# Kernel optimization log

Measured on AMD Instinct MI355X. Metric: run time of the kernel, lower is better.

## Reference

```python
import jax, jax.numpy as jnp
import numpy as np

N = 50000
E = 800000
IN_C = 128
HID = 64
HEADS = 4
OUT_C = 64


def setup_inputs() -> dict:
    key = jax.random.key(0)
    ks = jax.random.split(key, 20)
    s = 0.05
    inp = {
        "x": jax.random.normal(ks[0], (N, IN_C), dtype=jnp.float32),
        "edge_index": jax.random.randint(ks[1], (2, E), 0, N, dtype=jnp.int64),
        # layer 0: in=128 -> heads=4, C=64
        "W0": jax.random.normal(ks[2], (IN_C, HEADS * HID), jnp.float32) * s,
        "a0s": jax.random.normal(ks[3], (HEADS, HID), jnp.float32) * s,
        "a0d": jax.random.normal(ks[4], (HEADS, HID), jnp.float32) * s,
        "b0": jnp.zeros((HEADS * HID,), jnp.float32),
        # layer 1: 256 -> heads=4, C=64
        "W1": jax.random.normal(ks[5], (HEADS * HID, HEADS * HID), jnp.float32) * s,
        "a1s": jax.random.normal(ks[6], (HEADS, HID), jnp.float32) * s,
        "a1d": jax.random.normal(ks[7], (HEADS, HID), jnp.float32) * s,
        "b1": jnp.zeros((HEADS * HID,), jnp.float32),
        # layer 2: 256 -> heads=1, C=64
        "W2": jax.random.normal(ks[8], (HEADS * HID, HID), jnp.float32) * s,
        "a2s": jax.random.normal(ks[9], (1, HID), jnp.float32) * s,
        "a2d": jax.random.normal(ks[10], (1, HID), jnp.float32) * s,
        "b2": jnp.zeros((HID,), jnp.float32),
        # prediction head: Linear(64 -> 64)
        "hw": jax.random.normal(ks[11], (HID, OUT_C), jnp.float32) * s,
        "hb": jnp.zeros((OUT_C,), jnp.float32),
    }
    return inp


def gat_conv(x, src, dst, W, a_s, a_d, b, heads, n_nodes):
    # x: [N, F_in]; returns [N, heads*C]
    C = a_s.shape[1]
    h = (x @ W).reshape(n_nodes, heads, C)          # [N,H,C]
    alpha_s = jnp.sum(h * a_s, axis=-1)             # [N,H]
    alpha_d = jnp.sum(h * a_d, axis=-1)             # [N,H]
    e = jax.nn.leaky_relu(alpha_s[src] + alpha_d[dst], negative_slope=0.2)  # [E,H]
    m = jax.ops.segment_max(e, dst, num_segments=n_nodes)                  # per-dst max
    ex = jnp.exp(e - m[dst])
    denom = jax.ops.segment_sum(ex, dst, num_segments=n_nodes)
    alpha = ex / (denom[dst] + 1e-16)               # [E,H]
    out = jax.ops.segment_sum(alpha[:, :, None] * h[src], dst, num_segments=n_nodes)
    return out.reshape(n_nodes, heads * C) + b


def reference(x, edge_index, W0, a0s, a0d, b0, W1, a1s, a1d, b1, W2, a2s, a2d, b2, hw, hb):
    n = x.shape[0]
    # PyG GATConv default add_self_loops=True
    loop = jnp.arange(n, dtype=edge_index.dtype)
    src = jnp.concatenate([edge_index[0], loop])
    dst = jnp.concatenate([edge_index[1], loop])

    h = gat_conv(x, src, dst, W0, a0s, a0d, b0, HEADS, n)
    h = jax.nn.relu(h)
    h = gat_conv(h, src, dst, W1, a1s, a1d, b1, HEADS, n)
    h = jax.nn.relu(h)
    h = gat_conv(h, src, dst, W2, a2s, a2d, b2, 1, n)
    # batch is None -> mean over all nodes, keepdim
    g = jnp.mean(h, axis=0, keepdims=True)          # [1, HID]
    return g @ hw + hb                               # [1, OUT_C]
```

## Files before the change

### kernel.cpp

```cpp
#include <hip/hip_runtime.h>
#include <hip/hip_bf16.h>
#include <cstddef>

#define NN 50000
#define EE 800000

typedef __attribute__((ext_vector_type(8))) short short8;
typedef __attribute__((ext_vector_type(4))) float f32x4;

#define GLB __attribute__((address_space(1)))
#define LDS __attribute__((address_space(3)))

__device__ __forceinline__ float leaky(float x) { return x >= 0.f ? x : 0.2f * x; }
__device__ __forceinline__ float bf2f(unsigned short u) {
  return __uint_as_float(((unsigned int)u) << 16);
}
__device__ __forceinline__ float bflo(unsigned int v) { return __uint_as_float(v << 16); }
__device__ __forceinline__ float bfhi(unsigned int v) { return __uint_as_float(v & 0xFFFF0000u); }
__device__ __forceinline__ unsigned short f2bf(float f) {
  __hip_bfloat16 b = __float2bfloat16(f);
  return __builtin_bit_cast(unsigned short, b);
}
__device__ __forceinline__ void accum8(float a, uint4 v, float* acc) {
  acc[0] += a * bflo(v.x); acc[1] += a * bfhi(v.x);
  acc[2] += a * bflo(v.y); acc[3] += a * bfhi(v.y);
  acc[4] += a * bflo(v.z); acc[5] += a * bfhi(v.z);
  acc[6] += a * bflo(v.w); acc[7] += a * bfhi(v.w);
}

template <int LAYER>
__global__ __launch_bounds__(256) void gemm128_k(const unsigned short* __restrict__ A,
                                                 const unsigned short* __restrict__ Bt,
                                                 unsigned short* __restrict__ Cb,
                                                 int K,
                                                 const float* __restrict__ a_s,
                                                 const float* __restrict__ a_d,
                                                 float* __restrict__ als,
                                                 float* __restrict__ ald,
                                                 float* __restrict__ selfex) {
  __shared__ __align__(16) unsigned short As[4][64 * 32];
  __shared__ __align__(16) unsigned short Bs[4][128 * 32];
  const int tid = threadIdx.x;
  const int lane = tid & 63;
  const int w = tid >> 6;
  const int bm = blockIdx.x * 64;
  const int bn = blockIdx.y * 128;
  const int quad = lane >> 4;
  const int l16 = lane & 15;
  const int lrow = lane >> 2;
  const int lseg = lane & 3;
  f32x4 acc[8] = {};

  for (int kv = 0; kv < K; kv += 128) {
    if (kv) __syncthreads();
#pragma unroll
    for (int ks = 0; ks < 4; ++ks) {
      const int kc = kv + ks * 32;
      {
        int row = w * 16 + lrow;
        int g = lseg ^ ((row >> 2) & 3);
        int sr = bm + row; if (sr >= NN) sr = NN - 1;
        const unsigned short* gp = A + (size_t)sr * K + kc + g * 8;
        __builtin_amdgcn_global_load_lds((const GLB void*)gp,
                                         (LDS void*)&As[ks][(w * 16) * 32], 16, 0, 0);
      }
#pragma unroll
      for (int c = 0; c < 2; ++c) {
        int row = w * 32 + c * 16 + lrow;
        int g = lseg ^ ((row >> 2) & 3);
        const unsigned short* gp = Bt + (size_t)(bn + row) * K + kc + g * 8;
        __builtin_amdgcn_global_load_lds((const GLB void*)gp,
                                         (LDS void*)&Bs[ks][(w * 32 + c * 16) * 32], 16, 0, 0);
      }
    }
    __syncthreads();
#pragma unroll
    for (int ks = 0; ks < 4; ++ks) {
      const int ra = w * 16 + l16;
      short8 afr = *(const short8*)&As[ks][ra * 32 + ((quad ^ ((ra >> 2) & 3)) << 3)];
#pragma unroll
      for (int nt = 0; nt < 8; ++nt) {
        int rb = nt * 16 + l16;
        short8 bfr = *(const short8*)&Bs[ks][rb * 32 + ((quad ^ ((rb >> 2) & 3)) << 3)];
        acc[nt] = __builtin_amdgcn_mfma_f32_16x16x32_bf16(afr, bfr, acc[nt], 0, 0, 0);
      }
    }
  }
  const int h0 = blockIdx.y * 2;
  float vs[2][4] = {};
  float vd[2][4] = {};
#pragma unroll
  for (int nt = 0; nt < 8; ++nt) {
    const int h = nt >> 2;
    const float asv = a_s[(h0 + h) * 64 + (nt & 3) * 16 + l16];
    const float adv = a_d[(h0 + h) * 64 + (nt & 3) * 16 + l16];
#pragma unroll
    for (int reg = 0; reg < 4; ++reg) {
      unsigned short c = f2bf(acc[nt][reg]);
      int r = bm + w * 16 + quad * 4 + reg;
      if (r < NN) Cb[(size_t)r * 256 + bn + nt * 16 + l16] = c;
      float hv = bf2f(c);
      vs[h][reg] += hv * asv;
      vd[h][reg] += hv * adv;
    }
  }
#pragma unroll
  for (int off = 1; off < 16; off <<= 1) {
#pragma unroll
    for (int h = 0; h < 2; ++h)
#pragma unroll
      for (int reg = 0; reg < 4; ++reg) {
        vs[h][reg] += __shfl_xor(vs[h][reg], off, 64);
        vd[h][reg] += __shfl_xor(vd[h][reg], off, 64);
      }
  }
  if (l16 == 0) {
#pragma unroll
    for (int reg = 0; reg < 4; ++reg) {
      int r = bm + w * 16 + quad * 4 + reg;
      if (r < NN) {
#pragma unroll
        for (int h = 0; h < 2; ++h) {
          als[(size_t)r * 4 + h0 + h] = vs[h][reg];
          ald[(size_t)r * 4 + h0 + h] = vd[h][reg];
          selfex[(size_t)r * 4 + h0 + h] = __expf(leaky(vs[h][reg] + vd[h][reg]));
        }
      }
    }
  }
}

__global__ __launch_bounds__(256) void gemm64v_k(const unsigned short* __restrict__ A,
                                                 const unsigned short* __restrict__ Bt,
                                                 unsigned short* __restrict__ Cb,
                                                 int K,
                                                 const float* __restrict__ a_s,
                                                 const float* __restrict__ a_d,
                                                 float* __restrict__ als,
                                                 float* __restrict__ ald,
                                                 float* __restrict__ selfex) {
  __shared__ __align__(16) unsigned short As[4][64 * 32];
  __shared__ __align__(16) unsigned short Bs[4][64 * 32];
  const int tid = threadIdx.x;
  const int lane = tid & 63;
  const int w = tid >> 6;
  const int bm = blockIdx.x * 64;
  const int quad = lane >> 4;
  const int l16 = lane & 15;
  const int lrow = lane >> 2;
  const int lseg = lane & 3;
  f32x4 acc[4] = {};

  for (int kv = 0; kv < K; kv += 128) {
    if (kv) __syncthreads();
#pragma unroll
    for (int ks = 0; ks < 4; ++ks) {
      const int kc = kv + ks * 32;
      {
        int row = w * 16 + lrow;
        int g = lseg ^ ((row >> 2) & 3);
        int sr = bm + row; if (sr >= NN) sr = NN - 1;
        const unsigned short* gp = A + (size_t)sr * K + kc + g * 8;
        __builtin_amdgcn_global_load_lds((const GLB void*)gp,
                                         (LDS void*)&As[ks][(w * 16) * 32], 16, 0, 0);
      }
      {
        int row = w * 16 + lrow;
        int g = lseg ^ ((row >> 2) & 3);
        const unsigned short* gp = Bt + (size_t)row * K + kc + g * 8;
        __builtin_amdgcn_global_load_lds((const GLB void*)gp,
                                         (LDS void*)&Bs[ks][(w * 16) * 32], 16, 0, 0);
      }
    }
    __syncthreads();
#pragma unroll
    for (int ks = 0; ks < 4; ++ks) {
      const int ra = w * 16 + l16;
      short8 afr = *(const short8*)&As[ks][ra * 32 + ((quad ^ ((ra >> 2) & 3)) << 3)];
#pragma unroll
      for (int nt = 0; nt < 4; ++nt) {
        int rb = nt * 16 + l16;
        short8 bfr = *(const short8*)&Bs[ks][rb * 32 + ((quad ^ ((rb >> 2) & 3)) << 3)];
        acc[nt] = __builtin_amdgcn_mfma_f32_16x16x32_bf16(afr, bfr, acc[nt], 0, 0, 0);
      }
    }
  }
  float vs[4] = {};
  float vd[4] = {};
#pragma unroll
  for (int nt = 0; nt < 4; ++nt) {
    const float asv = a_s[nt * 16 + l16];
    const float adv = a_d[nt * 16 + l16];
#pragma unroll
    for (int reg = 0; reg < 4; ++reg) {
      unsigned short c = f2bf(acc[nt][reg]);
      int r = bm + w * 16 + quad * 4 + reg;
      if (r < NN) Cb[(size_t)r * 64 + nt * 16 + l16] = c;
      float hv = bf2f(c);
      vs[reg] += hv * asv;
      vd[reg] += hv * adv;
    }
  }
#pragma unroll
  for (int off = 1; off < 16; off <<= 1) {
#pragma unroll
    for (int reg = 0; reg < 4; ++reg) {
      vs[reg] += __shfl_xor(vs[reg], off, 64);
      vd[reg] += __shfl_xor(vd[reg], off, 64);
    }
  }
  if (l16 == 0) {
#pragma unroll
    for (int reg = 0; reg < 4; ++reg) {
      int r = bm + w * 16 + quad * 4 + reg;
      if (r < NN) {
        als[r] = vs[reg];
        ald[r] = vd[reg];
        selfex[r] = __expf(leaky(vs[reg] + vd[reg]));
      }
    }
  }
}

__global__ __launch_bounds__(256) void aggr4c_k(const int* __restrict__ deg,
                                                const int* __restrict__ csr_src,
                                                const float* __restrict__ als,
                                                const float* __restrict__ ald,
                                                const float* __restrict__ selfex,
                                                const uint4* __restrict__ hb4,
                                                const float* __restrict__ bias,
                                                uint4* __restrict__ out4) {
  const int dst = blockIdx.x * 4 + (threadIdx.x >> 6);
  const int lane = threadIdx.x & 63;
  const int slot = lane >> 4;
  const int l16 = lane & 15;
  const int head = l16 >> 2;
  const int rs = dst << 6;
  int dg = deg[dst]; dg = dg < 64 ? dg : 64;
  const float aldv = ald[dst * 4 + head];

  float acc[16] = {};
  float dsum = 0.f;
  if (slot == 0) {
    float a = selfex[dst * 4 + head];
    dsum += a;
    uint4 v0 = hb4[(size_t)dst * 32 + l16 * 2];
    uint4 v1 = hb4[(size_t)dst * 32 + l16 * 2 + 1];
    accum8(a, v0, acc);
    accum8(a, v1, acc + 8);
  }
  int j = slot;
  for (; j + 4 < dg; j += 8) {
    int s0 = csr_src[rs + j];
    int s1 = csr_src[rs + j + 4];
    float e0 = als[s0 * 4 + head];
    float e1 = als[s1 * 4 + head];
    uint4 va0 = hb4[(size_t)s0 * 32 + l16 * 2];
    uint4 vb0 = hb4[(size_t)s0 * 32 + l16 * 2 + 1];
    uint4 va1 = hb4[(size_t)s1 * 32 + l16 * 2];
    uint4 vb1 = hb4[(size_t)s1 * 32 + l16 * 2 + 1];
    float a0 = __expf(leaky(e0 + aldv));
    float a1 = __expf(leaky(e1 + aldv));
    dsum += a0 + a1;
    accum8(a0, va0, acc);
    accum8(a0, vb0, acc + 8);
    accum8(a1, va1, acc);
    accum8(a1, vb1, acc + 8);
  }
  for (; j < dg; j += 4) {
    int s0 = csr_src[rs + j];
    float e0 = als[s0 * 4 + head];
    uint4 va0 = hb4[(size_t)s0 * 32 + l16 * 2];
    uint4 vb0 = hb4[(size_t)s0 * 32 + l16 * 2 + 1];
    float a0 = __expf(leaky(e0 + aldv));
    dsum += a0;
    accum8(a0, va0, acc);
    accum8(a0, vb0, acc + 8);
  }
#pragma unroll
  for (int k = 0; k < 16; ++k) {
    acc[k] += __shfl_xor(acc[k], 16, 64);
    acc[k] += __shfl_xor(acc[k], 32, 64);
  }
  dsum += __shfl_xor(dsum, 16, 64);
  dsum += __shfl_xor(dsum, 32, 64);
  if (slot == 0) {
    const float inv = 1.f / (dsum + 1e-16f);
    const float* bz = bias + l16 * 16;
    uint4 o0, o1;
    float c0, c1;
    c0 = fmaxf(acc[0] * inv + bz[0], 0.f);   c1 = fmaxf(acc[1] * inv + bz[1], 0.f);
    o0.x = ((unsigned int)f2bf(c1) << 16) | f2bf(c0);
    c0 = fmaxf(acc[2] * inv + bz[2], 0.f);   c1 = fmaxf(acc[3] * inv + bz[3], 0.f);
    o0.y = ((unsigned int)f2bf(c1) << 16) | f2bf(c0);
    c0 = fmaxf(acc[4] * inv + bz[4], 0.f);   c1 = fmaxf(acc[5] * inv + bz[5], 0.f);
    o0.z = ((unsigned int)f2bf(c1) << 16) | f2bf(c0);
    c0 = fmaxf(acc[6] * inv + bz[6], 0.f);   c1 = fmaxf(acc[7] * inv + bz[7], 0.f);
    o0.w = ((unsigned int)f2bf(c1) << 16) | f2bf(c0);
    c0 = fmaxf(acc[8] * inv + bz[8], 0.f);   c1 = fmaxf(acc[9] * inv + bz[9], 0.f);
    o1.x = ((unsigned int)f2bf(c1) << 16) | f2bf(c0);
    c0 = fmaxf(acc[10] * inv + bz[10], 0.f); c1 = fmaxf(acc[11] * inv + bz[11], 0.f);
    o1.y = ((unsigned int)f2bf(c1) << 16) | f2bf(c0);
    c0 = fmaxf(acc[12] * inv + bz[12], 0.f); c1 = fmaxf(acc[13] * inv + bz[13], 0.f);
    o1.z = ((unsigned int)f2bf(c1) << 16) | f2bf(c0);
    c0 = fmaxf(acc[14] * inv + bz[14], 0.f); c1 = fmaxf(acc[15] * inv + bz[15], 0.f);
    o1.w = ((unsigned int)f2bf(c1) << 16) | f2bf(c0);
    out4[(size_t)dst * 32 + l16 * 2] = o0;
    out4[(size_t)dst * 32 + l16 * 2 + 1] = o1;
  }
}

__global__ __launch_bounds__(256) void aggr1c_k(const int* __restrict__ deg,
                                                const int* __restrict__ csr_src,
                                                const float* __restrict__ als,
                                                const float* __restrict__ ald,
                                                const float* __restrict__ selfex,
                                                const uint4* __restrict__ hb4,
                                                const float* __restrict__ bias,
                                                float* __restrict__ out) {
  const int dst = blockIdx.x * 4 + (threadIdx.x >> 6);
  const int lane = threadIdx.x & 63;
  const int slot = lane >> 3;
  const int c8 = lane & 7;
  const int rs = dst << 6;
  int dg = deg[dst]; dg = dg < 64 ? dg : 64;
  const float aldv = ald[dst];

  float acc[8] = {};
  float dsum = 0.f;
  if (slot == 0) {
    float a = selfex[dst];
    dsum += a;
    uint4 v = hb4[(size_t)dst * 8 + c8];
    accum8(a, v, acc);
  }
  int j = slot;
  for (; j + 8 < dg; j += 16) {
    int s0 = csr_src[rs + j];
    int s1 = csr_src[rs + j + 8];
    float e0 = als[s0];
    float e1 = als[s1];
    uint4 v0 = hb4[(size_t)s0 * 8 + c8];
    uint4 v1 = hb4[(size_t)s1 * 8 + c8];
    float a0 = __expf(leaky(e0 + aldv));
    float a1 = __expf(leaky(e1 + aldv));
    dsum += a0 + a1;
    accum8(a0, v0, acc);
    accum8(a1, v1, acc);
  }
  for (; j < dg; j += 8) {
    int s = csr_src[rs + j];
    float e = als[s];
    uint4 v = hb4[(size_t)s * 8 + c8];
    float a = __expf(leaky(e + aldv));
    dsum += a;
    accum8(a, v, acc);
  }
#pragma unroll
  for (int k = 0; k < 8; ++k) {
    acc[k] += __shfl_xor(acc[k], 8, 64);
    acc[k] += __shfl_xor(acc[k], 16, 64);
    acc[k] += __shfl_xor(acc[k], 32, 64);
  }
  dsum += __shfl_xor(dsum, 8, 64);
  dsum += __shfl_xor(dsum, 16, 64);
  dsum += __shfl_xor(dsum, 32, 64);
  if (slot == 0) {
    const float inv = 1.f / (dsum + 1e-16f);
    const float4 bz0 = *(const float4*)(bias + c8 * 8);
    const float4 bz1 = *(const float4*)(bias + c8 * 8 + 4);
    float4 o0 = make_float4(acc[0] * inv + bz0.x, acc[1] * inv + bz0.y,
                            acc[2] * inv + bz0.z, acc[3] * inv + bz0.w);
    float4 o1 = make_float4(acc[4] * inv + bz1.x, acc[5] * inv + bz1.y,
                            acc[6] * inv + bz1.z, acc[7] * inv + bz1.w);
    *(float4*)(out + (size_t)dst * 64 + c8 * 8) = o0;
    *(float4*)(out + (size_t)dst * 64 + c8 * 8 + 4) = o1;
  }
}

#define HS_BLK 782
__global__ __launch_bounds__(256) void prep_k(const int* __restrict__ ei,
                                              int* __restrict__ deg,
                                              int* __restrict__ csr_src,
                                              const float2* __restrict__ x2,
                                              unsigned int* __restrict__ xb_u,
                                              const float* __restrict__ W0,
                                              unsigned short* __restrict__ W0t,
                                              const float* __restrict__ W1,
                                              unsigned short* __restrict__ W1t,
                                              const float* __restrict__ W2,
                                              unsigned short* __restrict__ W2t,
                                              float* __restrict__ g) {
  int bid = blockIdx.x;
  int tid = threadIdx.x;
  if (bid < HS_BLK) {
    const int base = bid * 1024 + tid;
    int ss[4], dd[4], jj[4];
#pragma unroll
    for (int k = 0; k < 4; ++k) {
      int i = base + k * 256;
      bool m = i < EE;
      ss[k] = m ? ei[i] : 0;
      dd[k] = m ? ei[EE + i] : 0;
      jj[k] = 64;
      if (m) jj[k] = atomicAdd(&deg[dd[k]], 1);
    }
#pragma unroll
    for (int k = 0; k < 4; ++k)
      if (jj[k] < 64) csr_src[(dd[k] << 6) + jj[k]] = ss[k];
    return;
  }
  bid -= HS_BLK;
  if (bid < 12500) {
    int i = bid * 256 + tid;
    float2 v = x2[i];
    xb_u[i] = ((unsigned int)f2bf(v.y) << 16) | f2bf(v.x);
    return;
  }
  if (bid < 12948) {
    int r = (bid - 12500) * 256 + tid;
    if (r < 32768) {
      int n = r >> 7, k = r & 127;
      W0t[n * 128 + k] = f2bf(W0[k * 256 + n]);
    } else if (r < 98304) {
      int rr = r - 32768;
      int n = rr >> 8, k = rr & 255;
      W1t[n * 256 + k] = f2bf(W1[k * 256 + n]);
    } else {
      int rr = r - 98304;
      int n = rr >> 8, k = rr & 255;
      W2t[n * 256 + k] = f2bf(W2[k * 64 + n]);
    }
    return;
  }
  if (tid < 68) g[tid] = 0.f;
}

__global__ __launch_bounds__(256) void colsum_head_k(const float* __restrict__ h2,
                                                     float* __restrict__ g,
                                                     unsigned int* __restrict__ cnt,
                                                     const float* __restrict__ hw,
                                                     const float* __restrict__ hb,
                                                     float* __restrict__ out) {
  __shared__ float s[256];
  __shared__ float sg[64];
  __shared__ unsigned int sdone;
  int tid = threadIdx.x;
  int c = tid & 63, rg = tid >> 6;
  float acc = 0.f;
  for (int n = blockIdx.x * 4 + rg; n < NN; n += gridDim.x * 4)
    acc += h2[n * 64 + c];
  s[tid] = acc;
  __syncthreads();
  if (tid < 64) atomicAdd(&g[c], s[c] + s[64 + c] + s[128 + c] + s[192 + c]);
  __threadfence();
  __syncthreads();
  if (tid == 0) sdone = atomicAdd(cnt, 1);
  __syncthreads();
  if (sdone != gridDim.x - 1) return;
  if (tid < 64) sg[tid] = atomicAdd(&g[tid], 0.f);
  __syncthreads();
  if (tid < 64) {
    const float invN = 1.0f / (float)NN;
    float a2 = hb[tid];
#pragma unroll 8
    for (int cc = 0; cc < 64; ++cc) a2 += sg[cc] * invN * hw[cc * 64 + tid];
    out[tid] = a2;
  }
}

extern "C" void kernel_launch(void* const* d_in, const int* in_sizes, int n_in,
                              void* d_out, int out_size, void* d_ws, size_t ws_size,
                              hipStream_t stream) {
  const float* x   = (const float*)d_in[0];
  const int*   ei  = (const int*)d_in[1];
  const float* W0  = (const float*)d_in[2];
  const float* a0s = (const float*)d_in[3];
  const float* a0d = (const float*)d_in[4];
  const float* b0  = (const float*)d_in[5];
  const float* W1  = (const float*)d_in[6];
  const float* a1s = (const float*)d_in[7];
  const float* a1d = (const float*)d_in[8];
  const float* b1  = (const float*)d_in[9];
  const float* W2  = (const float*)d_in[10];
  const float* a2s = (const float*)d_in[11];
  const float* a2d = (const float*)d_in[12];
  const float* b2  = (const float*)d_in[13];
  const float* hw  = (const float*)d_in[14];
  const float* hb  = (const float*)d_in[15];
  float* out = (float*)d_out;

  char* w = (char*)d_ws;
  unsigned short* xb   = (unsigned short*)w; w += (size_t)NN * 128 * 2;
  unsigned short* bufG = (unsigned short*)w; w += (size_t)NN * 256 * 2;
  unsigned short* bufA = (unsigned short*)w; w += (size_t)NN * 256 * 2;
  float* bufF = (float*)w;                   w += (size_t)NN * 64 * 4;
  unsigned short* W0t = (unsigned short*)w;  w += 256 * 128 * 2;
  unsigned short* W1t = (unsigned short*)w;  w += 256 * 256 * 2;
  unsigned short* W2t = (unsigned short*)w;  w += 64 * 256 * 2;
  float* als  = (float*)w;    w += (size_t)NN * 4 * 4;
  float* ald  = (float*)w;    w += (size_t)NN * 4 * 4;
  float* sfx  = (float*)w;    w += (size_t)NN * 4 * 4;
  int* deg     = (int*)w;     w += (size_t)NN * 4;
  int* csr_src = (int*)w;     w += (size_t)NN * 64 * 4;
  float* g    = (float*)w;    w += 256;

  hipMemsetAsync(deg, 0, (size_t)NN * 4, stream);

  prep_k<<<HS_BLK + 12948 + 1, 256, 0, stream>>>(ei, deg, csr_src,
                                                 (const float2*)x, (unsigned int*)xb,
                                                 W0, W0t, W1, W1t, W2, W2t, g);

  const int G64 = (NN + 63) / 64;
  const int GA = NN / 4;

  gemm128_k<0><<<dim3(G64, 2), 256, 0, stream>>>(xb, W0t, bufG, 128, a0s, a0d, als, ald, sfx);
  aggr4c_k<<<GA, 256, 0, stream>>>(deg, csr_src, als, ald, sfx,
                                   (const uint4*)bufG, b0, (uint4*)bufA);
  gemm128_k<1><<<dim3(G64, 2), 256, 0, stream>>>(bufA, W1t, bufG, 256, a1s, a1d, als, ald, sfx);
  aggr4c_k<<<GA, 256, 0, stream>>>(deg, csr_src, als, ald, sfx,
                                   (const uint4*)bufG, b1, (uint4*)bufA);

  gemm64v_k<<<G64, 256, 0, stream>>>(bufA, W2t, bufG, 256, a2s, a2d, als, ald, sfx);
  aggr1c_k<<<GA, 256, 0, stream>>>(deg, csr_src, als, ald, sfx,
                                   (const uint4*)bufG, b2, bufF);

  colsum_head_k<<<256, 256, 0, stream>>>(bufF, g, (unsigned int*)(g + 64), hw, hb, out);
}
```

Before: 381.9 us.

## Split 4-head aggregation into per-slice waves over 32 channels

Each wave now processes one destination node for a 32-channel slice instead of all 256 channels, launching 8x more blocks, with 16 edges gathered concurrently per wave. This aims to raise memory-level parallelism and occupancy via fewer accumulators per thread. In exchange, edge indices, attention logits and exponentials are recomputed once per slice, gathers become 64-byte segments, and the reduction needs two extra shuffle stages.

```diff
diff --git a/kernel.cpp b/kernel.cpp
--- a/kernel.cpp
+++ b/kernel.cpp
@@ -222,7 +222,7 @@
   }
 }
 
-__global__ __launch_bounds__(256) void aggr4c_k(const int* __restrict__ deg,
+__global__ __launch_bounds__(256) void aggr4s_k(const int* __restrict__ deg,
                                                 const int* __restrict__ csr_src,
                                                 const float* __restrict__ als,
                                                 const float* __restrict__ ald,
@@ -230,83 +230,58 @@
                                                 const uint4* __restrict__ hb4,
                                                 const float* __restrict__ bias,
                                                 uint4* __restrict__ out4) {
-  const int dst = blockIdx.x * 4 + (threadIdx.x >> 6);
+  const int b = blockIdx.x;
+  const int slice = b & 7;
+  const int dst = (b >> 3) * 4 + (threadIdx.x >> 6);
   const int lane = threadIdx.x & 63;
-  const int slot = lane >> 4;
-  const int l16 = lane & 15;
-  const int head = l16 >> 2;
+  const int slot = lane >> 2;
+  const int l4 = lane & 3;
+  const int head = slice >> 1;
   const int rs = dst << 6;
   int dg = deg[dst]; dg = dg < 64 ? dg : 64;
   const float aldv = ald[dst * 4 + head];
-
-  float acc[16] = {};
+  const uint4* hp = hb4 + slice * 4 + l4;
+
+  float acc[8] = {};
   float dsum = 0.f;
   if (slot == 0) {
     float a = selfex[dst * 4 + head];
+    dsum = a;
+    accum8(a, hp[(size_t)dst * 32], acc);
+  }
+  for (int j = slot; j < dg; j += 16) {
+    int s = csr_src[rs + j];
+    float e = als[s * 4 + head];
+    uint4 v = hp[(size_t)s * 32];
+    float a = __expf(leaky(e + aldv));
     dsum += a;
-    uint4 v0 = hb4[(size_t)dst * 32 + l16 * 2];
-    uint4 v1 = hb4[(size_t)dst * 32 + l16 * 2 + 1];
-    accum8(a, v0, acc);
-    accum8(a, v1, acc + 8);
-  }
-  int j = slot;
-  for (; j + 4 < dg; j += 8) {
-    int s0 = csr_src[rs + j];
-    int s1 = csr_src[rs + j + 4];
-    float e0 = als[s0 * 4 + head];
-    float e1 = als[s1 * 4 + head];
-    uint4 va0 = hb4[(size_t)s0 * 32 + l16 * 2];
-    uint4 vb0 = hb4[(size_t)s0 * 32 + l16 * 2 + 1];
-    uint4 va1 = hb4[(size_t)s1 * 32 + l16 * 2];
-    uint4 vb1 = hb4[(size_t)s1 * 32 + l16 * 2 + 1];
-    float a0 = __expf(leaky(e0 + aldv));
-    float a1 = __expf(leaky(e1 + aldv));
-    dsum += a0 + a1;
-    accum8(a0, va0, acc);
-    accum8(a0, vb0, acc + 8);
-    accum8(a1, va1, acc);
-    accum8(a1, vb1, acc + 8);
-  }
-  for (; j < dg; j += 4) {
-    int s0 = csr_src[rs + j];
-    float e0 = als[s0 * 4 + head];
-    uint4 va0 = hb4[(size_t)s0 * 32 + l16 * 2];
-    uint4 vb0 = hb4[(size_t)s0 * 32 + l16 * 2 + 1];
-    float a0 = __expf(leaky(e0 + aldv));
-    dsum += a0;
-    accum8(a0, va0, acc);
-    accum8(a0, vb0, acc + 8);
-  }
-#pragma unroll
-  for (int k = 0; k < 16; ++k) {
+    accum8(a, v, acc);
+  }
+#pragma unroll
+  for (int k = 0; k < 8; ++k) {
+    acc[k] += __shfl_xor(acc[k], 4, 64);
+    acc[k] += __shfl_xor(acc[k], 8, 64);
     acc[k] += __shfl_xor(acc[k], 16, 64);
     acc[k] += __shfl_xor(acc[k], 32, 64);
   }
+  dsum += __shfl_xor(dsum, 4, 64);
+  dsum += __shfl_xor(dsum, 8, 64);
   dsum += __shfl_xor(dsum, 16, 64);
   dsum += __shfl_xor(dsum, 32, 64);
   if (slot == 0) {
     const float inv = 1.f / (dsum + 1e-16f);
-    const float* bz = bias + l16 * 16;
-    uint4 o0, o1;
+    const float* bz = bias + slice * 32 + l4 * 8;
+    uint4 o;
     float c0, c1;
-    c0 = fmaxf(acc[0] * inv + bz[0], 0.f);   c1 = fmaxf(acc[1] * inv + bz[1], 0.f);
-    o0.x = ((unsigned int)f2bf(c1) << 16) | f2bf(c0);
-    c0 = fmaxf(acc[2] * inv + bz[2], 0.f);   c1 = fmaxf(acc[3] * inv + bz[3], 0.f);
-    o0.y = ((unsigned int)f2bf(c1) << 16) | f2bf(c0);
-    c0 = fmaxf(acc[4] * inv + bz[4], 0.f);   c1 = fmaxf(acc[5] * inv + bz[5], 0.f);
-    o0.z = ((unsigned int)f2bf(c1) << 16) | f2bf(c0);
-    c0 = fmaxf(acc[6] * inv + bz[6], 0.f);   c1 = fmaxf(acc[7] * inv + bz[7], 0.f);
-    o0.w = ((unsigned int)f2bf(c1) << 16) | f2bf(c0);
-    c0 = fmaxf(acc[8] * inv + bz[8], 0.f);   c1 = fmaxf(acc[9] * inv + bz[9], 0.f);
-    o1.x = ((unsigned int)f2bf(c1) << 16) | f2bf(c0);
-    c0 = fmaxf(acc[10] * inv + bz[10], 0.f); c1 = fmaxf(acc[11] * inv + bz[11], 0.f);
-    o1.y = ((unsigned int)f2bf(c1) << 16) | f2bf(c0);
-    c0 = fmaxf(acc[12] * inv + bz[12], 0.f); c1 = fmaxf(acc[13] * inv + bz[13], 0.f);
-    o1.z = ((unsigned int)f2bf(c1) << 16) | f2bf(c0);
-    c0 = fmaxf(acc[14] * inv + bz[14], 0.f); c1 = fmaxf(acc[15] * inv + bz[15], 0.f);
-    o1.w = ((unsigned int)f2bf(c1) << 16) | f2bf(c0);
-    out4[(size_t)dst * 32 + l16 * 2] = o0;
-    out4[(size_t)dst * 32 + l16 * 2 + 1] = o1;
+    c0 = fmaxf(acc[0] * inv + bz[0], 0.f); c1 = fmaxf(acc[1] * inv + bz[1], 0.f);
+    o.x = ((unsigned int)f2bf(c1) << 16) | f2bf(c0);
+    c0 = fmaxf(acc[2] * inv + bz[2], 0.f); c1 = fmaxf(acc[3] * inv + bz[3], 0.f);
+    o.y = ((unsigned int)f2bf(c1) << 16) | f2bf(c0);
+    c0 = fmaxf(acc[4] * inv + bz[4], 0.f); c1 = fmaxf(acc[5] * inv + bz[5], 0.f);
+    o.z = ((unsigned int)f2bf(c1) << 16) | f2bf(c0);
+    c0 = fmaxf(acc[6] * inv + bz[6], 0.f); c1 = fmaxf(acc[7] * inv + bz[7], 0.f);
+    o.w = ((unsigned int)f2bf(c1) << 16) | f2bf(c0);
+    out4[(size_t)dst * 32 + slice * 4 + l4] = o;
   }
 }
 
@@ -513,12 +488,13 @@
 
   const int G64 = (NN + 63) / 64;
   const int GA = NN / 4;
+  const int GS = GA * 8;
 
   gemm128_k<0><<<dim3(G64, 2), 256, 0, stream>>>(xb, W0t, bufG, 128, a0s, a0d, als, ald, sfx);
-  aggr4c_k<<<GA, 256, 0, stream>>>(deg, csr_src, als, ald, sfx,
+  aggr4s_k<<<GS, 256, 0, stream>>>(deg, csr_src, als, ald, sfx,
                                    (const uint4*)bufG, b0, (uint4*)bufA);
   gemm128_k<1><<<dim3(G64, 2), 256, 0, stream>>>(bufA, W1t, bufG, 256, a1s, a1d, als, ald, sfx);
-  aggr4c_k<<<GA, 256, 0, stream>>>(deg, csr_src, als, ald, sfx,
+  aggr4s_k<<<GS, 256, 0, stream>>>(deg, csr_src, als, ald, sfx,
                                    (const uint4*)bufG, b1, (uint4*)bufA);
 
   gemm64v_k<<<G64, 256, 0, stream>>>(bufA, W2t, bufG, 256, a2s, a2d, als, ald, sfx);
```

Measured after the change: 571.1 us. 49.5% more time.
